# Kernel optimization log

Hardware: AMD Instinct MI355X
Metric: run time of the kernel (lower is better)

Reference implementation:

```python
import jax, jax.numpy as jnp
import numpy as np

B, OBS, DH, N, DK, DV, TASKS, OUT = 4096, 512, 1024, 8, 256, 1024, 10, 128
LOG_SIG_MIN, LOG_SIG_MAX = -20.0, 2.0


def _lin(k, fan_in, shape):
    return jax.random.normal(k, shape, jnp.float32) / np.sqrt(fan_in)


def setup_inputs() -> dict:
    ks = jax.random.split(jax.random.key(0), 18)
    return {
        "x": jax.random.normal(ks[0], (B, OBS), jnp.float32),
        "task_id": 3,
        # base MLP (2 layers)
        "Wb1": _lin(ks[1], OBS, (OBS, DH)), "bb1": jnp.zeros((DH,), jnp.float32),
        "Wb2": _lin(ks[2], DH, (DH, DH)), "bb2": jnp.zeros((DH,), jnp.float32),
        # per-expert MLPs (stacked over expert dim n)
        "We1": _lin(ks[3], DH, (N, DH, DH)), "be1": jnp.zeros((N, DH), jnp.float32),
        "We2": _lin(ks[4], DH, (N, DH, DH)), "be2": jnp.zeros((N, DH), jnp.float32),
        # per-expert attention v / k heads
        "Wv": _lin(ks[5], DH, (N, DH, DV)), "bv": jnp.zeros((N, DV), jnp.float32),
        "Wk": _lin(ks[6], DH, (N, DH, DK)), "bk": jnp.zeros((N, DK), jnp.float32),
        # per-task q networks (input = one-hot task vector of size TASKS)
        "Wq": _lin(ks[7], TASKS, (TASKS, TASKS, DK)), "bq": jnp.zeros((TASKS, DK), jnp.float32),
        # tower + last
        "Wt1": _lin(ks[8], DV, (DV, DH)), "bt1": jnp.zeros((DH,), jnp.float32),
        "Wl": _lin(ks[9], DH, (DH, OUT)) * 0.003, "bl": jnp.zeros((OUT,), jnp.float32),
    }


def reference(x, task_id, Wb1, bb1, Wb2, bb2, We1, be1, We2, be2,
              Wv, bv, Wk, bk, Wq, bq, Wt1, bt1, Wl, bl):
    act = jax.nn.relu
    # base: [B, DH]
    h = act(act(x @ Wb1 + bb1) @ Wb2 + bb2)
    # all experts at once: e [N, B, DH]
    e = act(jnp.einsum('bd,ndh->nbh', h, We1) + be1[:, None, :])
    e = act(jnp.einsum('nbd,ndh->nbh', e, We2) + be2[:, None, :])
    # attention values / keys per expert
    v = jnp.einsum('nbd,ndv->nbv', e, Wv) + bv[:, None, :]   # [N, B, DV]
    k = jnp.einsum('nbd,ndk->nbk', e, Wk) + bk[:, None, :]   # [N, B, DK]
    # q from one-hot task index through task-specific q net
    task_idx = jax.nn.one_hot(task_id, TASKS, dtype=x.dtype)  # [TASKS]
    q = task_idx @ Wq[task_id] + bq[task_id]                  # [DK]
    # raw (unnormalized) weights, as in the original (alphas are computed but unused)
    expkq = jnp.einsum('nbk,k->nb', k, q)                     # [N, B]
    res = jnp.einsum('nbv,nb->bv', v, expkq)                  # [B, DV]
    t = act(res @ Wt1 + bt1)
    out = t @ Wl + bl                                          # [B, OUT]
    mean, log_std = jnp.split(out, 2, axis=-1)
    log_std = jnp.clip(log_std, LOG_SIG_MIN, LOG_SIG_MAX)
    std = jnp.exp(log_std)
    return mean, std, log_std
```

## Files before the change

### kernel.cpp

```cpp
#include <hip/hip_runtime.h>
#include <hip/hip_bf16.h>

typedef unsigned short u16;
typedef unsigned int   u32;
typedef __attribute__((ext_vector_type(4))) float  f32x4;
typedef __attribute__((ext_vector_type(8))) __bf16 bf16x8;

#define B_    4096
#define OBS_  512
#define DH_   1024
#define NEXP_ 8
#define DK_   256
#define DV_   1024

__device__ __forceinline__ float b2f(u32 lo16) {
  return __builtin_bit_cast(float, lo16 << 16);
}
__device__ __forceinline__ u16 f2b(float f) {
  u32 u = __builtin_bit_cast(u32, f);
  return (u16)((u + 0x7fffu + ((u >> 16) & 1u)) >> 16);
}
__device__ __forceinline__ void gl_lds16(const u16* g, u16* l) {
  __builtin_amdgcn_global_load_lds(
      (__attribute__((address_space(1))) void*)(void*)g,
      (__attribute__((address_space(3))) void*)(void*)l,
      16, 0, 0);
}

__device__ __forceinline__ void tconv_body(const float* __restrict__ in,
                                           u16* __restrict__ outp,
                                           int R, int C, int rem, int tid) {
  __shared__ float tile[32][33];
  int gxs = (C == 128) ? 2 : 5;
  int c0 = (rem & ((1 << gxs) - 1)) * 32;
  int r0 = (rem >> gxs) * 32;
  int tx = tid & 31, ty = tid >> 5;
#pragma unroll
  for (int i = 0; i < 4; ++i)
    tile[ty + i * 8][tx] = in[(long)(r0 + ty + i * 8) * C + c0 + tx];
  __syncthreads();
#pragma unroll
  for (int i = 0; i < 4; ++i)
    outp[(long)(c0 + ty + i * 8) * R + r0 + tx] = f2b(tile[tx][ty + i * 8]);
}

__global__ __launch_bounds__(256)
void prep(const float* __restrict__ x,  u16* __restrict__ xb,
          const float* __restrict__ Wb1, u16* __restrict__ Wb1T,
          const float* __restrict__ Wb2, u16* __restrict__ Wb2T,
          const float* __restrict__ We1, u16* __restrict__ We1T,
          const float* __restrict__ We2, u16* __restrict__ We2T,
          const float* __restrict__ Wv,  u16* __restrict__ WvT,
          const float* __restrict__ Wt1, u16* __restrict__ Wt1T,
          const float* __restrict__ Wl,  u16* __restrict__ WlT,
          const float* __restrict__ Wq,  const float* __restrict__ bq,
          const float* __restrict__ bk,  const int* __restrict__ task,
          const float* __restrict__ Wk,  float* __restrict__ wnq,
          float* __restrict__ cn) {
  int tid = threadIdx.x;
  int bid = blockIdx.x;
  if (bid < 2048) {
    long i = ((long)bid * 256 + tid) * 4;
    float4 v = *(const float4*)(x + i);
    u16 o[4] = { f2b(v.x), f2b(v.y), f2b(v.z), f2b(v.w) };
    *(uint2*)(xb + i) = *(const uint2*)o;
    return;
  }
  bid -= 2048;
  if (bid < 512)  { tconv_body(Wb1, Wb1T, 512, 1024, bid, tid); return; }
  bid -= 512;
  if (bid < 1024) { tconv_body(Wb2, Wb2T, 1024, 1024, bid, tid); return; }
  bid -= 1024;
  if (bid < 8192) {
    int z = bid >> 10, rem = bid & 1023;
    tconv_body(We1 + (long)z * DH_ * DH_, We1T + (long)z * DH_ * DH_, 1024, 1024, rem, tid);
    return;
  }
  bid -= 8192;
  if (bid < 8192) {
    int z = bid >> 10, rem = bid & 1023;
    tconv_body(We2 + (long)z * DH_ * DH_, We2T + (long)z * DH_ * DH_, 1024, 1024, rem, tid);
    return;
  }
  bid -= 8192;
  if (bid < 8192) { tconv_body(Wv, WvT, 8192, 1024, bid, tid); return; }
  bid -= 8192;
  if (bid < 1024) { tconv_body(Wt1, Wt1T, 1024, 1024, bid, tid); return; }
  bid -= 1024;
  if (bid < 128)  { tconv_body(Wl, WlT, 1024, 128, bid, tid); return; }
  bid -= 128;
  int t = *task;
  const float* qrow = Wq + (long)(t * 10 + t) * DK_;
  const float* brow = bq + (long)t * DK_;
  int lane = tid & 63;
  if (bid < 2048) {
    int row = bid * 4 + (tid >> 6);
    const float* wr = Wk + (long)row * DK_;
    float s = 0.f;
#pragma unroll
    for (int i = 0; i < 4; ++i) {
      int j = lane + i * 64;
      s += wr[j] * (qrow[j] + brow[j]);
    }
    for (int off = 32; off; off >>= 1) s += __shfl_xor(s, off);
    if (lane == 0) wnq[row] = s;
  } else {
    int w = tid >> 6;
    for (int n = w; n < NEXP_; n += 4) {
      float s = 0.f;
#pragma unroll
      for (int i = 0; i < 4; ++i) {
        int j = lane + i * 64;
        s += bk[n * DK_ + j] * (qrow[j] + brow[j]);
      }
      for (int off = 32; off; off >>= 1) s += __shfl_xor(s, off);
      if (lane == 0) cn[n] = s;
    }
  }
}

template<int RELU, int OUT, int EKQ, int LDA, int LDB>
__global__ __launch_bounds__(256, 4)
void gemm_bt(const u16* __restrict__ A, const u16* __restrict__ Bt,
             const float* __restrict__ bias, void* __restrict__ Cv,
             int M, int N, int kper, int ksplit,
             long aB, long bB, long biasB, long cB,
             const float* __restrict__ wnq, float* __restrict__ ekqOut) {
  const int zz = blockIdx.z;
  const int split = zz % ksplit;
  const int batch = zz / ksplit;
  A  += (long)batch * aB + (long)split * kper;
  Bt += (long)batch * bB + (long)split * kper;

  int m_idx = blockIdx.y, n_idx = blockIdx.x;
  if (gridDim.x == 8) {
    int f = blockIdx.x + (blockIdx.y << 3);
    int xcd = f & 7, j = f >> 3;
    n_idx = j & 7;
    m_idx = (xcd << 2) | (j >> 3);
  }
  const int m0 = m_idx * 128, n0 = n_idx * 128;

  __shared__ u16 As[128 * 64];
  __shared__ u16 Bs[128 * 64];
  const int tid  = threadIdx.x;
  const int lane = tid & 63, wid = tid >> 6;
  const int wm = (wid >> 1) * 64, wn = (wid & 1) * 64;
  const int lr = lane & 15, quad = lane >> 4;
  const int srow = lane >> 3;
  const int scol = ((lane & 7) ^ srow) * 8;

  const u16* ap0 = A  + (long)(m0 + wid * 32 +  0 + srow) * LDA + scol;
  const u16* ap1 = A  + (long)(m0 + wid * 32 +  8 + srow) * LDA + scol;
  const u16* ap2 = A  + (long)(m0 + wid * 32 + 16 + srow) * LDA + scol;
  const u16* ap3 = A  + (long)(m0 + wid * 32 + 24 + srow) * LDA + scol;
  const u16* bp0 = Bt + (long)(n0 + wid * 32 +  0 + srow) * LDB + scol;
  const u16* bp1 = Bt + (long)(n0 + wid * 32 +  8 + srow) * LDB + scol;
  const u16* bp2 = Bt + (long)(n0 + wid * 32 + 16 + srow) * LDB + scol;
  const u16* bp3 = Bt + (long)(n0 + wid * 32 + 24 + srow) * LDB + scol;
  u16* la = &As[wid * 2048];
  u16* lb = &Bs[wid * 2048];

  const int rsw = lr & 7;
  const int aB0 = (wm + lr) * 64 + ((quad    ) ^ rsw) * 8;
  const int aB1 = (wm + lr) * 64 + ((quad + 4) ^ rsw) * 8;
  const int bB0 = (wn + lr) * 64 + ((quad    ) ^ rsw) * 8;
  const int bB1 = (wn + lr) * 64 + ((quad + 4) ^ rsw) * 8;

  f32x4 acc[4][4] = {};

  for (int k0 = 0; k0 < kper; k0 += 64) {
    __syncthreads();
    gl_lds16(ap0 + k0, la);        gl_lds16(ap1 + k0, la + 512);
    gl_lds16(ap2 + k0, la + 1024); gl_lds16(ap3 + k0, la + 1536);
    gl_lds16(bp0 + k0, lb);        gl_lds16(bp1 + k0, lb + 512);
    gl_lds16(bp2 + k0, lb + 1024); gl_lds16(bp3 + k0, lb + 1536);
    __syncthreads();
#pragma unroll
    for (int h = 0; h < 2; ++h) {
      const int ab = h ? aB1 : aB0, bb = h ? bB1 : bB0;
      bf16x8 af[4], bfr[4];
#pragma unroll
      for (int i = 0; i < 4; ++i) af[i]  = *(const bf16x8*)(&As[ab + i * 1024]);
#pragma unroll
      for (int i = 0; i < 4; ++i) bfr[i] = *(const bf16x8*)(&Bs[bb + i * 1024]);
#pragma unroll
      for (int mi = 0; mi < 4; ++mi)
#pragma unroll
        for (int ni = 0; ni < 4; ++ni)
          acc[mi][ni] = __builtin_amdgcn_mfma_f32_16x16x32_bf16(af[mi], bfr[ni], acc[mi][ni], 0, 0, 0);
    }
  }

  if (OUT == 1) {
    float* C = (float*)Cv + (long)split * ((long)M * N);
#pragma unroll
    for (int mi = 0; mi < 4; ++mi)
#pragma unroll
      for (int ni = 0; ni < 4; ++ni) {
        int col = n0 + wn + ni * 16 + lr;
#pragma unroll
        for (int r = 0; r < 4; ++r) {
          int row = m0 + wm + mi * 16 + quad * 4 + r;
          C[(long)row * N + col] = acc[mi][ni][r];
        }
      }
  } else {
    u16* C = (u16*)Cv + (long)batch * cB;
    const float* bptr = bias ? bias + (long)batch * biasB : nullptr;
#pragma unroll
    for (int mi = 0; mi < 4; ++mi) {
      float psum[4] = {0.f, 0.f, 0.f, 0.f};
#pragma unroll
      for (int ni = 0; ni < 4; ++ni) {
        int col = n0 + wn + ni * 16 + lr;
        float bcol = bptr ? bptr[col] : 0.f;
        float wq = EKQ ? wnq[(long)batch * N + col] : 0.f;
#pragma unroll
        for (int r = 0; r < 4; ++r) {
          int row = m0 + wm + mi * 16 + quad * 4 + r;
          float v = acc[mi][ni][r] + bcol;
          if (RELU) v = fmaxf(v, 0.f);
          C[(long)row * N + col] = f2b(v);
          if (EKQ) psum[r] += v * wq;
        }
      }
      if (EKQ) {
#pragma unroll
        for (int r = 0; r < 4; ++r) {
          float s = psum[r];
          s += __shfl_xor(s, 1); s += __shfl_xor(s, 2);
          s += __shfl_xor(s, 4); s += __shfl_xor(s, 8);
          if (lr == 0)
            atomicAdd(ekqOut + (long)batch * M + (m0 + wm + mi * 16 + quad * 4 + r), s);
        }
      }
    }
  }
}

__global__ __launch_bounds__(256)
void reduce2_relu(const float* __restrict__ part, const float* __restrict__ bias,
                  u16* __restrict__ outp, int N, long stride) {
  long f4 = ((long)blockIdx.x * 256 + threadIdx.x) * 4;
  float4 v0 = *(const float4*)(part + f4);
  float4 v1 = *(const float4*)(part + stride + f4);
  int col = (int)(f4 % N);
  float4 bb = *(const float4*)(bias + col);
  u16 o[4];
  o[0] = f2b(fmaxf(v0.x + v1.x + bb.x, 0.f));
  o[1] = f2b(fmaxf(v0.y + v1.y + bb.y, 0.f));
  o[2] = f2b(fmaxf(v0.z + v1.z + bb.z, 0.f));
  o[3] = f2b(fmaxf(v0.w + v1.w + bb.w, 0.f));
  *(uint2*)(outp + f4) = *(const uint2*)o;
}

__global__ __launch_bounds__(256)
void reduce_res(const u16* __restrict__ y, const float* __restrict__ ekq,
                const float* __restrict__ cn, const float* __restrict__ bvp,
                u16* __restrict__ res) {
  long f8 = ((long)blockIdx.x * 256 + threadIdx.x) * 8;
  int b = (int)(f8 >> 10);
  int v = (int)(f8 & (DV_ - 1));
  float acc[8] = {};
#pragma unroll
  for (int n = 0; n < NEXP_; ++n) {
    float s = ekq[n * B_ + b] + cn[n];
    uint4 p = *(const uint4*)(y + ((long)(n * B_ + b) * DV_) + v);
    const u32* pi = (const u32*)&p;
    float4 b0 = *(const float4*)(bvp + n * DV_ + v);
    float4 b1 = *(const float4*)(bvp + n * DV_ + v + 4);
    acc[0] += s * (b2f(pi[0] & 0xffffu) + b0.x);
    acc[1] += s * (b2f(pi[0] >> 16)     + b0.y);
    acc[2] += s * (b2f(pi[1] & 0xffffu) + b0.z);
    acc[3] += s * (b2f(pi[1] >> 16)     + b0.w);
    acc[4] += s * (b2f(pi[2] & 0xffffu) + b1.x);
    acc[5] += s * (b2f(pi[2] >> 16)     + b1.y);
    acc[6] += s * (b2f(pi[3] & 0xffffu) + b1.z);
    acc[7] += s * (b2f(pi[3] >> 16)     + b1.w);
  }
  u16 o[8];
#pragma unroll
  for (int i = 0; i < 8; ++i) o[i] = f2b(acc[i]);
  *(uint4*)(res + f8) = *(const uint4*)o;
}

__global__ __launch_bounds__(256)
void reduce_final(const float* __restrict__ part, const float* __restrict__ bl,
                  float* __restrict__ outp) {
  int flat = blockIdx.x * 256 + threadIdx.x;
  int c = flat & 127, b = flat >> 7;
  float v = bl[c];
  const long S = (long)B_ * 128;
#pragma unroll
  for (int s = 0; s < 8; ++s) v += part[s * S + flat];
  if (c < 64) {
    outp[b * 64 + c] = v;
  } else {
    int i = b * 64 + (c - 64);
    float ls = fminf(fmaxf(v, -20.f), 2.f);
    outp[262144 + i] = expf(ls);
    outp[524288 + i] = ls;
  }
}

extern "C" void kernel_launch(void* const* d_in, const int* in_sizes, int n_in,
                              void* d_out, int out_size, void* d_ws, size_t ws_size,
                              hipStream_t stream) {
  const float* x   = (const float*)d_in[0];
  const int*   task= (const int*)  d_in[1];
  const float* Wb1 = (const float*)d_in[2];
  const float* bb1 = (const float*)d_in[3];
  const float* Wb2 = (const float*)d_in[4];
  const float* bb2 = (const float*)d_in[5];
  const float* We1 = (const float*)d_in[6];
  const float* be1 = (const float*)d_in[7];
  const float* We2 = (const float*)d_in[8];
  const float* be2 = (const float*)d_in[9];
  const float* Wv  = (const float*)d_in[10];
  const float* bv  = (const float*)d_in[11];
  const float* Wk  = (const float*)d_in[12];
  const float* bk  = (const float*)d_in[13];
  const float* Wq  = (const float*)d_in[14];
  const float* bq  = (const float*)d_in[15];
  const float* Wt1 = (const float*)d_in[16];
  const float* bt1 = (const float*)d_in[17];
  const float* Wl  = (const float*)d_in[18];
  const float* bl  = (const float*)d_in[19];
  float* outp = (float*)d_out;

  char* ws = (char*)d_ws;
  size_t off = 0;
  auto alloc = [&](size_t bytes) -> char* {
    char* p = ws + off;
    off += (bytes + 255) & ~(size_t)255;
    return p;
  };

  u16* xb    = (u16*)alloc((size_t)B_ * OBS_ * 2);
  u16* Wb1T  = (u16*)alloc((size_t)DH_ * OBS_ * 2);
  u16* Wb2T  = (u16*)alloc((size_t)DH_ * DH_ * 2);
  u16* We1T  = (u16*)alloc((size_t)NEXP_ * DH_ * DH_ * 2);
  u16* We2T  = (u16*)alloc((size_t)NEXP_ * DH_ * DH_ * 2);
  u16* WvT   = (u16*)alloc((size_t)DV_ * NEXP_ * DH_ * 2);
  u16* Wt1T  = (u16*)alloc((size_t)DH_ * DV_ * 2);
  u16* WlT   = (u16*)alloc((size_t)128 * DH_ * 2);
  u16* h1    = (u16*)alloc((size_t)B_ * DH_ * 2);
  u16* h     = (u16*)alloc((size_t)B_ * DH_ * 2);
  u16* e1    = (u16*)alloc((size_t)NEXP_ * B_ * DH_ * 2);
  u16* e2    = (u16*)alloc((size_t)NEXP_ * B_ * DH_ * 2);
  float* cn  = (float*)alloc(NEXP_ * 4);
  float* wnq = (float*)alloc((size_t)NEXP_ * DH_ * 4);
  float* ekq = (float*)alloc((size_t)NEXP_ * B_ * 4);
  float* partA = (float*)e1;
  u16*   y     = e1;
  u16*   res   = h1;
  u16*   tt    = h;
  float* partB = (float*)e2;

  hipMemsetAsync(ekq, 0, (size_t)NEXP_ * B_ * 4, stream);
  prep<<<31361, 256, 0, stream>>>(x, xb, Wb1, Wb1T, Wb2, Wb2T, We1, We1T,
                                  We2, We2T, Wv, WvT, Wt1, Wt1T, Wl, WlT,
                                  Wq, bq, bk, task, Wk, wnq, cn);

  const long S1 = (long)B_ * DH_;
  gemm_bt<0, 1, 0, OBS_, OBS_><<<dim3(8, 32, 2), 256, 0, stream>>>(xb, Wb1T, nullptr, partA,
      B_, DH_, 256, 2, 0, 0, 0, 0, nullptr, nullptr);
  reduce2_relu<<<4096, 256, 0, stream>>>(partA, bb1, h1, DH_, S1);
  gemm_bt<0, 1, 0, DH_, DH_><<<dim3(8, 32, 2), 256, 0, stream>>>(h1, Wb2T, nullptr, partA,
      B_, DH_, 512, 2, 0, 0, 0, 0, nullptr, nullptr);
  reduce2_relu<<<4096, 256, 0, stream>>>(partA, bb2, h, DH_, S1);
  gemm_bt<1, 0, 0, DH_, DH_><<<dim3(8, 32, 8), 256, 0, stream>>>(h, We1T, be1, e1,
      B_, DH_, DH_, 1, 0, (long)DH_ * DH_, DH_, (long)B_ * DH_, nullptr, nullptr);
  gemm_bt<1, 0, 1, DH_, DH_><<<dim3(8, 32, 8), 256, 0, stream>>>(e1, We2T, be2, e2,
      B_, DH_, DH_, 1, (long)B_ * DH_, (long)DH_ * DH_, DH_, (long)B_ * DH_, wnq, ekq);
  gemm_bt<0, 0, 0, DH_, NEXP_ * DH_><<<dim3(8, 32, 8), 256, 0, stream>>>(e2, WvT, nullptr, y,
      B_, DV_, DH_, 1, (long)B_ * DH_, DH_, 0, (long)B_ * DV_, nullptr, nullptr);
  reduce_res<<<2048, 256, 0, stream>>>(y, ekq, cn, bv, res);
  gemm_bt<0, 1, 0, DV_, DV_><<<dim3(8, 32, 2), 256, 0, stream>>>(res, Wt1T, nullptr, partB,
      B_, DH_, 512, 2, 0, 0, 0, 0, nullptr, nullptr);
  reduce2_relu<<<4096, 256, 0, stream>>>(partB, bt1, tt, DH_, S1);
  gemm_bt<0, 1, 0, DH_, DH_><<<dim3(1, 32, 8), 256, 0, stream>>>(tt, WlT, nullptr, partB,
      B_, 128, 128, 8, 0, 0, 0, 0, nullptr, nullptr);
  reduce_final<<<(B_ * 128) / 256, 256, 0, stream>>>(partB, bl, outp);
}
```

Measured before the change: 494.4 us.

## Replace split-K GEMMs with 64-row tile GEMM fusing bias+ReLU; drop ekq atomics

Adds a gemm_sm kernel that uses 64x128 tiles without split-K for the three dense 4096x1024 layers, and applies bias and ReLU in its epilogue. This removes the fp32 partial-sum writes and the separate reduce2_relu passes. The ekq reduction in the expert GEMM now sums per block in LDS and writes per-n-tile partials instead of using global atomics, which also drops the memset. reduce_res then sums the 8 partials per expert. The cost is more blocks with smaller tiles, lower per-block reuse, and a little extra LDS synchronisation.

```diff
diff --git a/kernel.cpp b/kernel.cpp
--- a/kernel.cpp
+++ b/kernel.cpp
@@ -125,7 +125,7 @@
              const float* __restrict__ bias, void* __restrict__ Cv,
              int M, int N, int kper, int ksplit,
              long aB, long bB, long biasB, long cB,
-             const float* __restrict__ wnq, float* __restrict__ ekqOut) {
+             const float* __restrict__ wnq, float* __restrict__ ekqPart) {
   const int zz = blockIdx.z;
   const int split = zz % ksplit;
   const int batch = zz / ksplit;
@@ -208,6 +208,8 @@
   } else {
     u16* C = (u16*)Cv + (long)batch * cB;
     const float* bptr = bias ? bias + (long)batch * biasB : nullptr;
+    float* eLds = (float*)As;
+    if (EKQ) __syncthreads();
 #pragma unroll
     for (int mi = 0; mi < 4; ++mi) {
       float psum[4] = {0.f, 0.f, 0.f, 0.f};
@@ -231,53 +233,125 @@
           float s = psum[r];
           s += __shfl_xor(s, 1); s += __shfl_xor(s, 2);
           s += __shfl_xor(s, 4); s += __shfl_xor(s, 8);
-          if (lr == 0)
-            atomicAdd(ekqOut + (long)batch * M + (m0 + wm + mi * 16 + quad * 4 + r), s);
+          if (lr == 0) eLds[wid * 64 + mi * 16 + quad * 4 + r] = s;
         }
       }
     }
-  }
+    if (EKQ) {
+      __syncthreads();
+      if (tid < 128) {
+        int half = tid >> 6, loc = tid & 63;
+        float v = eLds[half * 128 + loc] + eLds[half * 128 + 64 + loc];
+        ekqPart[((long)batch * 8 + n_idx) * M + m0 + tid] = v;
+      }
+    }
+  }
+}
+
+template<int LDA, int LDB>
+__global__ __launch_bounds__(256, 4)
+void gemm_sm(const u16* __restrict__ A, const u16* __restrict__ Bt,
+             const float* __restrict__ bias, u16* __restrict__ C,
+             int N, int kper) {
+  int f = blockIdx.x + (blockIdx.y << 3);
+  int xcd = f & 7;
+  const int n_idx = (f >> 3) & 7;
+  const int m_idx = (xcd << 3) | (f >> 6);
+  const int m0 = m_idx * 64, n0 = n_idx * 128;
+
+  __shared__ u16 As[64 * 64];
+  __shared__ u16 Bs[128 * 64];
+  const int tid  = threadIdx.x;
+  const int lane = tid & 63, wid = tid >> 6;
+  const int wn = wid * 32;
+  const int lr = lane & 15, quad = lane >> 4;
+  const int srow = lane >> 3;
+  const int scol = ((lane & 7) ^ srow) * 8;
+
+  const u16* ap0 = A  + (long)(m0 + wid * 16 + 0 + srow) * LDA + scol;
+  const u16* ap1 = A  + (long)(m0 + wid * 16 + 8 + srow) * LDA + scol;
+  const u16* bp0 = Bt + (long)(n0 + wid * 32 +  0 + srow) * LDB + scol;
+  const u16* bp1 = Bt + (long)(n0 + wid * 32 +  8 + srow) * LDB + scol;
+  const u16* bp2 = Bt + (long)(n0 + wid * 32 + 16 + srow) * LDB + scol;
+  const u16* bp3 = Bt + (long)(n0 + wid * 32 + 24 + srow) * LDB + scol;
+  u16* la = &As[wid * 1024];
+  u16* lb = &Bs[wid * 2048];
+
+  const int rsw = lr & 7;
+  const int aB0 = lr * 64 + ((quad    ) ^ rsw) * 8;
+  const int aB1 = lr * 64 + ((quad + 4) ^ rsw) * 8;
+  const int bB0 = (wn + lr) * 64 + ((quad    ) ^ rsw) * 8;
+  const int bB1 = (wn + lr) * 64 + ((quad + 4) ^ rsw) * 8;
+
+  f32x4 acc[4][2] = {};
+
+  for (int k0 = 0; k0 < kper; k0 += 64) {
+    __syncthreads();
+    gl_lds16(ap0 + k0, la);        gl_lds16(ap1 + k0, la + 512);
+    gl_lds16(bp0 + k0, lb);        gl_lds16(bp1 + k0, lb + 512);
+    gl_lds16(bp2 + k0, lb + 1024); gl_lds16(bp3 + k0, lb + 1536);
+    __syncthreads();
+#pragma unroll
+    for (int h = 0; h < 2; ++h) {
+      const int ab = h ? aB1 : aB0, bb = h ? bB1 : bB0;
+      bf16x8 af[4], bfr[2];
+#pragma unroll
+      for (int i = 0; i < 4; ++i) af[i]  = *(const bf16x8*)(&As[ab + i * 1024]);
+#pragma unroll
+      for (int i = 0; i < 2; ++i) bfr[i] = *(const bf16x8*)(&Bs[bb + i * 1024]);
+#pragma unroll
+      for (int mi = 0; mi < 4; ++mi)
+#pragma unroll
+        for (int ni = 0; ni < 2; ++ni)
+          acc[mi][ni] = __builtin_amdgcn_mfma_f32_16x16x32_bf16(af[mi], bfr[ni], acc[mi][ni], 0, 0, 0);
+    }
+  }
+
+#pragma unroll
+  for (int mi = 0; mi < 4; ++mi)
+#pragma unroll
+    for (int ni = 0; ni < 2; ++ni) {
+      int col = n0 + wn + ni * 16 + lr;
+      float bcol = bias[col];
+#pragma unroll
+      for (int r = 0; r < 4; ++r) {
+        int row = m0 + mi * 16 + quad * 4 + r;
+        C[(long)row * N + col] = f2b(fmaxf(acc[mi][ni][r] + bcol, 0.f));
+      }
+    }
 }
 
 __global__ __launch_bounds__(256)
-void reduce2_relu(const float* __restrict__ part, const float* __restrict__ bias,
-                  u16* __restrict__ outp, int N, long stride) {
-  long f4 = ((long)blockIdx.x * 256 + threadIdx.x) * 4;
-  float4 v0 = *(const float4*)(part + f4);
-  float4 v1 = *(const float4*)(part + stride + f4);
-  int col = (int)(f4 % N);
-  float4 bb = *(const float4*)(bias + col);
-  u16 o[4];
-  o[0] = f2b(fmaxf(v0.x + v1.x + bb.x, 0.f));
-  o[1] = f2b(fmaxf(v0.y + v1.y + bb.y, 0.f));
-  o[2] = f2b(fmaxf(v0.z + v1.z + bb.z, 0.f));
-  o[3] = f2b(fmaxf(v0.w + v1.w + bb.w, 0.f));
-  *(uint2*)(outp + f4) = *(const uint2*)o;
-}
-
-__global__ __launch_bounds__(256)
-void reduce_res(const u16* __restrict__ y, const float* __restrict__ ekq,
+void reduce_res(const u16* __restrict__ y, const float* __restrict__ ekqPart,
                 const float* __restrict__ cn, const float* __restrict__ bvp,
                 u16* __restrict__ res) {
   long f8 = ((long)blockIdx.x * 256 + threadIdx.x) * 8;
   int b = (int)(f8 >> 10);
   int v = (int)(f8 & (DV_ - 1));
+  float s[NEXP_];
+#pragma unroll
+  for (int n = 0; n < NEXP_; ++n) {
+    float t = cn[n];
+#pragma unroll
+    for (int nt = 0; nt < 8; ++nt) t += ekqPart[((long)n * 8 + nt) * B_ + b];
+    s[n] = t;
+  }
   float acc[8] = {};
 #pragma unroll
   for (int n = 0; n < NEXP_; ++n) {
-    float s = ekq[n * B_ + b] + cn[n];
+    float sn = s[n];
     uint4 p = *(const uint4*)(y + ((long)(n * B_ + b) * DV_) + v);
     const u32* pi = (const u32*)&p;
     float4 b0 = *(const float4*)(bvp + n * DV_ + v);
     float4 b1 = *(const float4*)(bvp + n * DV_ + v + 4);
-    acc[0] += s * (b2f(pi[0] & 0xffffu) + b0.x);
-    acc[1] += s * (b2f(pi[0] >> 16)     + b0.y);
-    acc[2] += s * (b2f(pi[1] & 0xffffu) + b0.z);
-    acc[3] += s * (b2f(pi[1] >> 16)     + b0.w);
-    acc[4] += s * (b2f(pi[2] & 0xffffu) + b1.x);
-    acc[5] += s * (b2f(pi[2] >> 16)     + b1.y);
-    acc[6] += s * (b2f(pi[3] & 0xffffu) + b1.z);
-    acc[7] += s * (b2f(pi[3] >> 16)     + b1.w);
+    acc[0] += sn * (b2f(pi[0] & 0xffffu) + b0.x);
+    acc[1] += sn * (b2f(pi[0] >> 16)     + b0.y);
+    acc[2] += sn * (b2f(pi[1] & 0xffffu) + b0.z);
+    acc[3] += sn * (b2f(pi[1] >> 16)     + b0.w);
+    acc[4] += sn * (b2f(pi[2] & 0xffffu) + b1.x);
+    acc[5] += sn * (b2f(pi[2] >> 16)     + b1.y);
+    acc[6] += sn * (b2f(pi[3] & 0xffffu) + b1.z);
+    acc[7] += sn * (b2f(pi[3] >> 16)     + b1.w);
   }
   u16 o[8];
 #pragma unroll
@@ -351,35 +425,26 @@
   u16* e2    = (u16*)alloc((size_t)NEXP_ * B_ * DH_ * 2);
   float* cn  = (float*)alloc(NEXP_ * 4);
   float* wnq = (float*)alloc((size_t)NEXP_ * DH_ * 4);
-  float* ekq = (float*)alloc((size_t)NEXP_ * B_ * 4);
-  float* partA = (float*)e1;
+  float* ekqPart = (float*)alloc((size_t)NEXP_ * 8 * B_ * 4);
   u16*   y     = e1;
   u16*   res   = h1;
   u16*   tt    = h;
   float* partB = (float*)e2;
 
-  hipMemsetAsync(ekq, 0, (size_t)NEXP_ * B_ * 4, stream);
   prep<<<31361, 256, 0, stream>>>(x, xb, Wb1, Wb1T, Wb2, Wb2T, We1, We1T,
                                   We2, We2T, Wv, WvT, Wt1, Wt1T, Wl, WlT,
                                   Wq, bq, bk, task, Wk, wnq, cn);
 
-  const long S1 = (long)B_ * DH_;
-  gemm_bt<0, 1, 0, OBS_, OBS_><<<dim3(8, 32, 2), 256, 0, stream>>>(xb, Wb1T, nullptr, partA,
-      B_, DH_, 256, 2, 0, 0, 0, 0, nullptr, nullptr);
-  reduce2_relu<<<4096, 256, 0, stream>>>(partA, bb1, h1, DH_, S1);
-  gemm_bt<0, 1, 0, DH_, DH_><<<dim3(8, 32, 2), 256, 0, stream>>>(h1, Wb2T, nullptr, partA,
-      B_, DH_, 512, 2, 0, 0, 0, 0, nullptr, nullptr);
-  reduce2_relu<<<4096, 256, 0, stream>>>(partA, bb2, h, DH_, S1);
+  gemm_sm<OBS_, OBS_><<<dim3(8, 64), 256, 0, stream>>>(xb, Wb1T, bb1, h1, DH_, OBS_);
+  gemm_sm<DH_, DH_><<<dim3(8, 64), 256, 0, stream>>>(h1, Wb2T, bb2, h, DH_, DH_);
   gemm_bt<1, 0, 0, DH_, DH_><<<dim3(8, 32, 8), 256, 0, stream>>>(h, We1T, be1, e1,
       B_, DH_, DH_, 1, 0, (long)DH_ * DH_, DH_, (long)B_ * DH_, nullptr, nullptr);
   gemm_bt<1, 0, 1, DH_, DH_><<<dim3(8, 32, 8), 256, 0, stream>>>(e1, We2T, be2, e2,
-      B_, DH_, DH_, 1, (long)B_ * DH_, (long)DH_ * DH_, DH_, (long)B_ * DH_, wnq, ekq);
+      B_, DH_, DH_, 1, (long)B_ * DH_, (long)DH_ * DH_, DH_, (long)B_ * DH_, wnq, ekqPart);
   gemm_bt<0, 0, 0, DH_, NEXP_ * DH_><<<dim3(8, 32, 8), 256, 0, stream>>>(e2, WvT, nullptr, y,
       B_, DV_, DH_, 1, (long)B_ * DH_, DH_, 0, (long)B_ * DV_, nullptr, nullptr);
-  reduce_res<<<2048, 256, 0, stream>>>(y, ekq, cn, bv, res);
-  gemm_bt<0, 1, 0, DV_, DV_><<<dim3(8, 32, 2), 256, 0, stream>>>(res, Wt1T, nullptr, partB,
-      B_, DH_, 512, 2, 0, 0, 0, 0, nullptr, nullptr);
-  reduce2_relu<<<4096, 256, 0, stream>>>(partB, bt1, tt, DH_, S1);
+  reduce_res<<<2048, 256, 0, stream>>>(y, ekqPart, cn, bv, res);
+  gemm_sm<DV_, DV_><<<dim3(8, 64), 256, 0, stream>>>(res, Wt1T, bt1, tt, DH_, DV_);
   gemm_bt<0, 1, 0, DH_, DH_><<<dim3(1, 32, 8), 256, 0, stream>>>(tt, WlT, nullptr, partB,
       B_, 128, 128, 8, 0, 0, 0, 0, nullptr, nullptr);
   reduce_final<<<(B_ * 128) / 256, 256, 0, stream>>>(partB, bl, outp);
```

Measured after the change: 458.0 us. -7.4%, faster.
